# Performance work log

Measured on AMD Instinct MI355X. Metric: run time of the kernel, lower is better.

The kernel has to match this reference:

```python
import jax, jax.numpy as jnp
import numpy as np

DIM, HEADS, DEPTH, SEQ, LOCAL_W = 1024, 16, 7, 2048, 64
HEAD_DIM = DIM // HEADS
SCALE = 1.0 / HEAD_DIM ** 0.5


def cantor_mask(S, depth, local_window):
    """Allowed (i,j): |i-j| within local window, OR |i-j| lies in the Cantor set
    under `depth` levels of ternary subdivision (no base-3 digit equals 1)."""
    idx = np.arange(S)
    d = np.abs(idx[:, None] - idx[None, :])
    x = d.copy()
    ok = np.ones_like(d, dtype=bool)
    for _ in range(depth):
        ok &= (x % 3) != 1
        x //= 3
    ok &= x == 0  # offset must be < 3**depth
    return jnp.asarray(ok | (d <= local_window))  # [S, S] bool


def setup_inputs() -> dict:
    key = jax.random.key(0)
    ks = jax.random.split(key, 8)
    B = 2
    s = 0.02
    return {
        "query": jax.random.normal(ks[0], (B, SEQ, DIM), jnp.float32),
        "key_value": jax.random.normal(ks[1], (B, SEQ, DIM), jnp.float32),
        "Wq": jax.random.normal(ks[2], (DIM, DIM), jnp.float32) * s,
        "bq": jnp.zeros((DIM,), jnp.float32),
        "Wkv": jax.random.normal(ks[3], (DIM, 2 * DIM), jnp.float32) * s,
        "bkv": jnp.zeros((2 * DIM,), jnp.float32),
        "Wo": jax.random.normal(ks[4], (DIM, DIM), jnp.float32) * s,
        "bo": jnp.zeros((DIM,), jnp.float32),
    }


def reference(query, key_value, Wq, bq, Wkv, bkv, Wo, bo):
    B, S, D = query.shape
    H, hd = HEADS, HEAD_DIM
    mask = cantor_mask(S, DEPTH, LOCAL_W)  # static [S, S] bool

    q = (query @ Wq + bq).reshape(B, S, H, hd).transpose(0, 2, 1, 3)  # [B,H,S,hd]
    kv = (key_value @ Wkv + bkv).reshape(B, S, 2, H, hd).transpose(2, 0, 3, 1, 4)
    k, v = kv[0], kv[1]  # [B,H,S,hd]

    scores = jnp.einsum("bhqd,bhkd->bhqk", q, k) * SCALE
    scores = jnp.where(mask, scores, jnp.finfo(scores.dtype).min)
    attn = jax.nn.softmax(scores, axis=-1)
    out = jnp.einsum("bhqk,bhkd->bhqd", attn, v)  # [B,H,S,hd]
    out = out.transpose(0, 2, 1, 3).reshape(B, S, D)
    return out @ Wo + bo
```

## Files before the change

### kernel.cpp

```cpp
#include <hip/hip_runtime.h>
#include <stdint.h>

typedef _Float16 half_t;
typedef __attribute__((ext_vector_type(8))) _Float16 half8;
typedef __attribute__((ext_vector_type(4))) _Float16 half4;
typedef __attribute__((ext_vector_type(4))) float floatx4;

#define SEQ 2048
#define NH 16
#define HD 64

#define MFMA16(a, b, c) __builtin_amdgcn_mfma_f32_16x16x16f16(a, b, c, 0, 0, 0)
#define MFMA32K(a, b, c) __builtin_amdgcn_mfma_f32_16x16x32_f16(a, b, c, 0, 0, 0)

#define QSCALE 0.1803368801111306f

__global__ __launch_bounds__(256) void prep(
    const float* __restrict__ query, const float* __restrict__ key_value,
    const float* __restrict__ Wq, const float* __restrict__ Wkv,
    const float* __restrict__ Wo, half_t* __restrict__ xq,
    half_t* __restrict__ xkv, half_t* __restrict__ wqT,
    half_t* __restrict__ wkvT, half_t* __restrict__ woT,
    uint8_t* __restrict__ tok, uint8_t* __restrict__ tok16,
    uint64_t* __restrict__ maskw) {
  int bx = blockIdx.x, tid = threadIdx.x;
  if (bx < 2048) {
    const float* s; half_t* d; int base;
    if (bx < 1024) { s = query; d = xq; base = bx * 4096; }
    else { s = key_value; d = xkv; base = (bx - 1024) * 4096; }
#pragma unroll
    for (int u = 0; u < 4; ++u) {
      int i = base + u * 1024 + tid * 4;
      floatx4 v = *(const floatx4*)(s + i);
      half4 h;
      h[0] = (half_t)v[0]; h[1] = (half_t)v[1];
      h[2] = (half_t)v[2]; h[3] = (half_t)v[3];
      *(half4*)(d + i) = h;
    }
    return;
  }
  if (bx < 4096) {
    __shared__ float tile[32][33];
    int tx = tid & 31, ty = tid >> 5;
    const int K = 1024;
#pragma unroll
    for (int u = 0; u < 2; ++u) {
      int t = (bx - 2048) * 2 + u;
      const float* W; half_t* Wt; int N, nt, kt;
      if (t < 1024) { W = Wq; Wt = wqT; N = 1024; nt = t & 31; kt = t >> 5; }
      else if (t < 3072) { int t2 = t - 1024; W = Wkv; Wt = wkvT; N = 2048; nt = t2 & 63; kt = t2 >> 6; }
      else { int t2 = t - 3072; W = Wo; Wt = woT; N = 1024; nt = t2 & 31; kt = t2 >> 5; }
      int n0 = nt * 32, k0 = kt * 32;
#pragma unroll
      for (int i = 0; i < 4; ++i)
        tile[ty + i * 8][tx] = W[(size_t)(k0 + ty + i * 8) * N + n0 + tx];
      __syncthreads();
#pragma unroll
      for (int i = 0; i < 4; ++i)
        Wt[(size_t)(n0 + ty + i * 8) * K + k0 + tx] = (half_t)tile[tx][ty + i * 8];
      __syncthreads();
    }
    return;
  }
  __shared__ uint8_t slut[2048];
  int ib = bx - 4096;
  for (int d = tid; d < 2048; d += 256) {
    int x = d;
    bool ok = true;
    for (int it = 0; it < 7; ++it) { ok &= ((x % 3) != 1); x /= 3; }
    ok &= (x == 0);
    slut[d] = (ok || d <= 64) ? 1 : 0;
  }
  __syncthreads();
  if (ib == 0) {
    if (tid < 64) {
      int delta = tid - 32;
      int lo = delta * 64 - 63, hi = delta * 64 + 63;
      uint8_t any = 0;
      for (int x = lo; x <= hi; ++x) {
        int a = x < 0 ? -x : x;
        if (a < 2048) any |= slut[a];
      }
      tok[tid] = any;
    }
    {
      int d16 = tid - 128;
      int ctr = d16 * 16;
      uint8_t any = 0;
      for (int x = ctr - 15; x <= ctr + 15; ++x) {
        int a = x < 0 ? -x : x;
        if (a < 2048) any |= slut[a];
      }
      tok16[tid] = any;
    }
  }
  int g = ib * 256 + tid;
  int tt = g - 2048;
  uint64_t w = 0;
  for (int jj = 0; jj < 64; ++jj) {
    int d = tt - jj; d = d < 0 ? -d : d;
    if (d < 2048 && slut[d]) w |= (1ull << jj);
  }
  maskw[g] = w;
}

__device__ __forceinline__ void cp16(half_t* lds, const half_t* g) {
  __builtin_amdgcn_global_load_lds(
      (const __attribute__((address_space(1))) uint32_t*)g,
      (__attribute__((address_space(3))) uint32_t*)lds, 16, 0, 0);
}

__global__ __launch_bounds__(256) void gemm_qkv(
    const half_t* __restrict__ xq, const half_t* __restrict__ xkv,
    const half_t* __restrict__ wqT, const half_t* __restrict__ wkvT,
    const float* __restrict__ bq, const float* __restrict__ bkv,
    half_t* __restrict__ qout, half_t* __restrict__ kout,
    half_t* __restrict__ vTout) {
  extern __shared__ char smemraw[];
  half_t* As = (half_t*)smemraw;
  half_t* Bs = As + 8192;
  const int K = 1024;
  bool isq = blockIdx.y < 8;
  const half_t* A = isq ? xq : xkv;
  const half_t* Bt = isq ? wqT : wkvT;
  const float* bias = isq ? bq : bkv;
  int n0 = (isq ? blockIdx.y : (blockIdx.y - 8)) * 128;
  int m0 = blockIdx.x * 128;

  int tid = threadIdx.x;
  int wave = tid >> 6, lane = tid & 63;
  int c = lane & 15, quad = lane >> 4;
  int wm = (wave >> 1) * 64, wn = (wave & 1) * 64;

  floatx4 acc[4][4] = {};
  int arow = tid >> 2, akc = (tid & 3) * 8;

  cp16(&As[wave * 512], A + (size_t)(m0 + arow) * K + akc);
  cp16(&As[2048 + wave * 512], A + (size_t)(m0 + 64 + arow) * K + akc);
  cp16(&Bs[wave * 512], Bt + (size_t)(n0 + arow) * K + akc);
  cp16(&Bs[2048 + wave * 512], Bt + (size_t)(n0 + 64 + arow) * K + akc);

  for (int kt = 0; kt < 32; ++kt) {
    __syncthreads();
    if (kt + 1 < 32) {
      int k0 = (kt + 1) * 32;
      int b = (kt + 1) & 1;
      cp16(&As[b * 4096 + wave * 512], A + (size_t)(m0 + arow) * K + k0 + akc);
      cp16(&As[b * 4096 + 2048 + wave * 512], A + (size_t)(m0 + 64 + arow) * K + k0 + akc);
      cp16(&Bs[b * 4096 + wave * 512], Bt + (size_t)(n0 + arow) * K + k0 + akc);
      cp16(&Bs[b * 4096 + 2048 + wave * 512], Bt + (size_t)(n0 + 64 + arow) * K + k0 + akc);
    }
    int b = kt & 1;
    half8 af[4], bf[4];
#pragma unroll
    for (int mt = 0; mt < 4; ++mt)
      af[mt] = *(const half8*)&As[b * 4096 + (wm + mt * 16 + c) * 32 + quad * 8];
#pragma unroll
    for (int nt = 0; nt < 4; ++nt)
      bf[nt] = *(const half8*)&Bs[b * 4096 + (wn + nt * 16 + c) * 32 + quad * 8];
#pragma unroll
    for (int mt = 0; mt < 4; ++mt)
#pragma unroll
      for (int nt = 0; nt < 4; ++nt)
        acc[mt][nt] = MFMA32K(af[mt], bf[nt], acc[mt][nt]);
  }

  __syncthreads();
  half_t* ep = (half_t*)smemraw;
  int bb = m0 >> 11, sbase = m0 & 2047;
  bool isv = (!isq) && (n0 >= 1024);

  if (!isv) {
#pragma unroll
    for (int nt = 0; nt < 4; ++nt) {
      int nl = wn + nt * 16 + c;
      float bv = bias[n0 + nl];
#pragma unroll
      for (int mt = 0; mt < 4; ++mt)
#pragma unroll
        for (int r = 0; r < 4; ++r) {
          int ml = wm + mt * 16 + quad * 4 + r;
          float v = acc[mt][nt][r] + bv;
          if (isq) v *= QSCALE;
          ep[ml * 128 + nl] = (half_t)v;
        }
    }
    __syncthreads();
    half_t* outp = isq ? qout : kout;
#pragma unroll
    for (int rd = 0; rd < 8; ++rd) {
      int id = rd * 256 + tid;
      int ml = id >> 4, ch = id & 15;
      int ng = n0 + ch * 8;
      int h = ng >> 6, d0 = ng & 63;
      half8 v = *(const half8*)&ep[ml * 128 + ch * 8];
      *(half8*)(outp + ((size_t)(bb * 16 + h) * SEQ + sbase + ml) * 64 + d0) = v;
    }
  } else {
#pragma unroll
    for (int nt = 0; nt < 4; ++nt) {
      int nl = wn + nt * 16 + c;
      float bv = bias[n0 + nl];
#pragma unroll
      for (int mt = 0; mt < 4; ++mt) {
        int ml = wm + mt * 16 + quad * 4;
        half4 hv;
#pragma unroll
        for (int r = 0; r < 4; ++r) hv[r] = (half_t)(acc[mt][nt][r] + bv);
        *(half4*)&ep[nl * 136 + ml] = hv;
      }
    }
    __syncthreads();
#pragma unroll
    for (int rd = 0; rd < 8; ++rd) {
      int id = rd * 256 + tid;
      int nl = id >> 4, mc = id & 15;
      int ng = n0 + nl;
      int h = (ng >> 6) & 15, d = ng & 63;
      half8 v = *(const half8*)&ep[nl * 136 + mc * 8];
      *(half8*)(vTout + ((size_t)(bb * 16 + h) * 64 + d) * SEQ + sbase + mc * 8) = v;
    }
  }
}

__global__ __launch_bounds__(256) void gemm_out(
    const half_t* __restrict__ A, const half_t* __restrict__ Bt,
    const float* __restrict__ bias, float* __restrict__ outf) {
  __shared__ half_t As[2][128 * 32];
  __shared__ half_t Bs[2][64 * 32];
  const int K = 1024;
  int tid = threadIdx.x;
  int wave = tid >> 6, lane = tid & 63;
  int c = lane & 15, quad = lane >> 4;
  int wm = (wave >> 1) * 64, wn = (wave & 1) * 32;
  int m0 = blockIdx.x * 128, n0 = blockIdx.y * 64;

  floatx4 acc[4][2] = {};
  int arow = tid >> 2, akc = (tid & 3) * 8;

  cp16(&As[0][wave * 512], A + (size_t)(m0 + arow) * K + akc);
  cp16(&As[0][2048 + wave * 512], A + (size_t)(m0 + 64 + arow) * K + akc);
  cp16(&Bs[0][wave * 512], Bt + (size_t)(n0 + arow) * K + akc);

  for (int kt = 0; kt < 32; ++kt) {
    __syncthreads();
    if (kt + 1 < 32) {
      int k0 = (kt + 1) * 32;
      int b = (kt + 1) & 1;
      cp16(&As[b][wave * 512], A + (size_t)(m0 + arow) * K + k0 + akc);
      cp16(&As[b][2048 + wave * 512], A + (size_t)(m0 + 64 + arow) * K + k0 + akc);
      cp16(&Bs[b][wave * 512], Bt + (size_t)(n0 + arow) * K + k0 + akc);
    }
    int b = kt & 1;
    half8 af[4], bf[2];
#pragma unroll
    for (int mt = 0; mt < 4; ++mt)
      af[mt] = *(const half8*)&As[b][(wm + mt * 16 + c) * 32 + quad * 8];
#pragma unroll
    for (int nt = 0; nt < 2; ++nt)
      bf[nt] = *(const half8*)&Bs[b][(wn + nt * 16 + c) * 32 + quad * 8];
#pragma unroll
    for (int mt = 0; mt < 4; ++mt)
#pragma unroll
      for (int nt = 0; nt < 2; ++nt)
        acc[mt][nt] = MFMA32K(af[mt], bf[nt], acc[mt][nt]);
  }

#pragma unroll
  for (int nt = 0; nt < 2; ++nt) {
    int n = n0 + wn + nt * 16 + c;
    float bv = bias[n];
#pragma unroll
    for (int mt = 0; mt < 4; ++mt)
#pragma unroll
      for (int r = 0; r < 4; ++r) {
        int m = m0 + wm + mt * 16 + quad * 4 + r;
        outf[(size_t)m * 1024 + n] = acc[mt][nt][r] + bv;
      }
  }
}

__global__ __launch_bounds__(512) void attn_kernel(
    const half_t* __restrict__ qb, const half_t* __restrict__ kb,
    const half_t* __restrict__ vTg, half_t* __restrict__ ctx,
    const uint64_t* __restrict__ maskw, const uint8_t* __restrict__ tok,
    const uint8_t* __restrict__ tok16g) {
  __shared__ half_t kT[64 * 64];
  __shared__ half_t vT[64 * 64];
  __shared__ half_t ot[128 * 72];
  __shared__ int list[34];
  __shared__ uint8_t tok16s[256];

  int tid = threadIdx.x, wave = tid >> 6, lane = tid & 63;
  int c = lane & 15, q = lane >> 4;
  int id = blockIdx.x;
  int bh = (id & 7) * 4 + ((id >> 3) & 3);
  int it128 = id >> 5;
  int i0 = it128 << 7;
  const half_t* qbase = qb + (size_t)bh * SEQ * HD;
  const half_t* kg = kb + (size_t)bh * SEQ * HD;
  const half_t* vg = vTg + (size_t)bh * HD * SEQ;

  if (tid < 256) tok16s[tid] = tok16g[tid];
  if (wave == 0) {
    int jt = lane;
    int base = i0 >> 6;
    bool act = (jt < 32) &&
               (tok[(jt - base) + 32] | tok[(jt - base - 1) + 32]);
    unsigned long long bal = __ballot(act);
    if (act) {
      int pre = __popcll(bal & ((1ull << jt) - 1));
      list[1 + pre] = jt << 6;
    }
    if (lane == 0) list[0] = __popcll(bal);
  }

  int i_row = i0 + wave * 16 + c;
  int it16 = (i0 >> 4) + wave;
  half8 qf0 = *(const half8*)(qbase + (size_t)i_row * 64 + q * 8);
  half8 qf1 = *(const half8*)(qbase + (size_t)i_row * 64 + 32 + q * 8);

  floatx4 oacc[4] = {};
  floatx4 lacc = {};
  half4 ones;
  ones[0] = (half_t)1.f; ones[1] = (half_t)1.f;
  ones[2] = (half_t)1.f; ones[3] = (half_t)1.f;

  int srow = tid >> 3;
  int sch = tid & 7;
  int ssw = srow & 7;

  __syncthreads();
  int nact = list[0];
  int j0 = list[1];

  half8 kr = *(const half8*)(kg + (size_t)(j0 + srow) * 64 + sch * 8);
  half8 vr = *(const half8*)(vg + (size_t)srow * SEQ + j0 + sch * 8);

  for (int ti = 0; ti < nact; ++ti) {
    uint64_t w = maskw[(i_row - j0) + 2048];
    int bidx = (j0 >> 4) - it16 + 128;
    __syncthreads();
    *(half8*)&kT[srow * 64 + ((sch ^ ssw) * 8)] = kr;
    *(half8*)&vT[srow * 64 + ((sch ^ ssw) * 8)] = vr;
    int j0n = j0;
    if (ti + 1 < nact) {
      j0n = list[2 + ti];
      kr = *(const half8*)(kg + (size_t)(j0n + srow) * 64 + sch * 8);
      vr = *(const half8*)(vg + (size_t)srow * SEQ + j0n + sch * 8);
    }
    __syncthreads();

    uint32_t wlo = (uint32_t)(w >> (4 * q));
    uint32_t whi = (uint32_t)(w >> (32 + 4 * q));
#pragma unroll
    for (int jt = 0; jt < 4; ++jt) {
      if (!tok16s[bidx + jt]) continue;
      int row = jt * 16 + c;
      int sw = c & 7;
      half8 a0 = *(const half8*)&kT[row * 64 + ((q ^ sw) * 8)];
      half8 a1 = *(const half8*)&kT[row * 64 + (((4 + q) ^ sw) * 8)];
      floatx4 t = {};
      t = MFMA32K(a0, qf0, t);
      t = MFMA32K(a1, qf1, t);
      uint32_t ww = (jt < 2) ? wlo : whi;
#pragma unroll
      for (int r = 0; r < 4; ++r) {
        float p = __builtin_exp2f(t[r]);
        int bitpos = 16 * (jt & 1) + r;
        uint32_t msk = (uint32_t)(((int)(ww << (31 - bitpos))) >> 31);
        t[r] = __uint_as_float(__float_as_uint(p) & msk);
      }
      auto lo = __builtin_amdgcn_cvt_pkrtz(t[0], t[1]);
      auto hi = __builtin_amdgcn_cvt_pkrtz(t[2], t[3]);
      half4 pb;
      pb[0] = lo[0]; pb[1] = lo[1]; pb[2] = hi[0]; pb[3] = hi[1];
      lacc = MFMA16(ones, pb, lacc);
#pragma unroll
      for (int mt = 0; mt < 4; ++mt) {
        int drow = mt * 16 + c;
        int ch = 2 * jt + (q >> 1);
        half4 a = *(const half4*)&vT[drow * 64 + ((ch ^ sw) * 8) + (q & 1) * 4];
        oacc[mt] = MFMA16(a, pb, oacc[mt]);
      }
    }
    j0 = j0n;
  }

  float inv_l = 1.0f / lacc[0];
#pragma unroll
  for (int mt = 0; mt < 4; ++mt)
#pragma unroll
    for (int r = 0; r < 4; ++r)
      ot[(wave * 16 + c) * 72 + mt * 16 + 4 * q + r] = (half_t)(oacc[mt][r] * inv_l);
  __syncthreads();
  {
    int row = tid >> 2, chq = tid & 3;
    int b = bh >> 4, h = bh & 15;
    size_t base = (((size_t)(b * SEQ + i0 + row) * NH) + h) * 64 + chq * 16;
    half8 v0 = *(const half8*)&ot[row * 72 + chq * 16];
    half8 v1 = *(const half8*)&ot[row * 72 + chq * 16 + 8];
    *(half8*)(ctx + base) = v0;
    *(half8*)(ctx + base + 8) = v1;
  }
}

extern "C" void kernel_launch(void* const* d_in, const int* in_sizes, int n_in,
                              void* d_out, int out_size, void* d_ws, size_t ws_size,
                              hipStream_t stream) {
  const float* query = (const float*)d_in[0];
  const float* key_value = (const float*)d_in[1];
  const float* Wq = (const float*)d_in[2];
  const float* bq = (const float*)d_in[3];
  const float* Wkv = (const float*)d_in[4];
  const float* bkv = (const float*)d_in[5];
  const float* Wo = (const float*)d_in[6];
  const float* bo = (const float*)d_in[7];

  char* ws = (char*)d_ws;
  uint8_t* tok = (uint8_t*)ws;
  uint8_t* tok16 = (uint8_t*)(ws + 1024);
  uint64_t* maskw = (uint64_t*)(ws + 4096);
  const size_t MB = 1ull << 20;
  half_t* xq = (half_t*)(ws + 1 * MB);
  half_t* xkv = (half_t*)(ws + 9 * MB);
  half_t* wqT = (half_t*)(ws + 17 * MB);
  half_t* wkvT = (half_t*)(ws + 19 * MB);
  half_t* woT = (half_t*)(ws + 23 * MB);
  half_t* qbuf = (half_t*)(ws + 25 * MB);
  half_t* kbuf = (half_t*)(ws + 33 * MB);
  half_t* vTg = (half_t*)(ws + 41 * MB);
  half_t* ctx = xq;

  hipLaunchKernelGGL(prep, dim3(4112), dim3(256), 0, stream,
                     query, key_value, Wq, Wkv, Wo, xq, xkv, wqT, wkvT, woT,
                     tok, tok16, maskw);
  hipLaunchKernelGGL(gemm_qkv, dim3(32, 24), dim3(256), 34816, stream,
                     xq, xkv, wqT, wkvT, bq, bkv, qbuf, kbuf, vTg);
  hipLaunchKernelGGL(attn_kernel, dim3(512), dim3(512), 0, stream,
                     qbuf, kbuf, vTg, ctx, maskw, tok, tok16);
  hipLaunchKernelGGL(gemm_out, dim3(32, 16), dim3(256), 0, stream,
                     ctx, woT, bo, (float*)d_out);
}
```

Measured before the change: 218.1 us.

## Swizzle GEMM LDS tiles and double-buffer K/V tiles in attention

The two GEMM kernels XOR-swizzle the 16-byte chunk position within each 32-half LDS row, on both the async copy side and the fragment-read side, to reduce LDS bank conflicts. The attention kernel gets two K and V shared-memory buffers and prefetches two tiles ahead in registers. This cuts the per-tile barriers from two to one, so the next tile's LDS store can overlap the current tile's MFMA work. The cost is twice the LDS for K/V (lower occupancy possible) and extra registers for the second prefetch set.

Result: no change. 216.9 us (-0.6%).

```diff
diff --git a/kernel.cpp b/kernel.cpp
--- a/kernel.cpp
+++ b/kernel.cpp
@@ -133,7 +133,9 @@
   int wm = (wave >> 1) * 64, wn = (wave & 1) * 64;
 
   floatx4 acc[4][4] = {};
-  int arow = tid >> 2, akc = (tid & 3) * 8;
+  int arow = tid >> 2;
+  int akc = ((tid & 3) ^ (arow & 3)) * 8;
+  int csw = c & 3;
 
   cp16(&As[wave * 512], A + (size_t)(m0 + arow) * K + akc);
   cp16(&As[2048 + wave * 512], A + (size_t)(m0 + 64 + arow) * K + akc);
@@ -154,10 +156,10 @@
     half8 af[4], bf[4];
 #pragma unroll
     for (int mt = 0; mt < 4; ++mt)
-      af[mt] = *(const half8*)&As[b * 4096 + (wm + mt * 16 + c) * 32 + quad * 8];
+      af[mt] = *(const half8*)&As[b * 4096 + (wm + mt * 16 + c) * 32 + ((quad ^ csw) * 8)];
 #pragma unroll
     for (int nt = 0; nt < 4; ++nt)
-      bf[nt] = *(const half8*)&Bs[b * 4096 + (wn + nt * 16 + c) * 32 + quad * 8];
+      bf[nt] = *(const half8*)&Bs[b * 4096 + (wn + nt * 16 + c) * 32 + ((quad ^ csw) * 8)];
 #pragma unroll
     for (int mt = 0; mt < 4; ++mt)
 #pragma unroll
@@ -236,7 +238,9 @@
   int m0 = blockIdx.x * 128, n0 = blockIdx.y * 64;
 
   floatx4 acc[4][2] = {};
-  int arow = tid >> 2, akc = (tid & 3) * 8;
+  int arow = tid >> 2;
+  int akc = ((tid & 3) ^ (arow & 3)) * 8;
+  int csw = c & 3;
 
   cp16(&As[0][wave * 512], A + (size_t)(m0 + arow) * K + akc);
   cp16(&As[0][2048 + wave * 512], A + (size_t)(m0 + 64 + arow) * K + akc);
@@ -255,10 +259,10 @@
     half8 af[4], bf[2];
 #pragma unroll
     for (int mt = 0; mt < 4; ++mt)
-      af[mt] = *(const half8*)&As[b][(wm + mt * 16 + c) * 32 + quad * 8];
+      af[mt] = *(const half8*)&As[b][(wm + mt * 16 + c) * 32 + ((quad ^ csw) * 8)];
 #pragma unroll
     for (int nt = 0; nt < 2; ++nt)
-      bf[nt] = *(const half8*)&Bs[b][(wn + nt * 16 + c) * 32 + quad * 8];
+      bf[nt] = *(const half8*)&Bs[b][(wn + nt * 16 + c) * 32 + ((quad ^ csw) * 8)];
 #pragma unroll
     for (int mt = 0; mt < 4; ++mt)
 #pragma unroll
@@ -285,8 +289,8 @@
     const half_t* __restrict__ vTg, half_t* __restrict__ ctx,
     const uint64_t* __restrict__ maskw, const uint8_t* __restrict__ tok,
     const uint8_t* __restrict__ tok16g) {
-  __shared__ half_t kT[64 * 64];
-  __shared__ half_t vT[64 * 64];
+  __shared__ half_t kT[2][64 * 64];
+  __shared__ half_t vT[2][64 * 64];
   __shared__ half_t ot[128 * 72];
   __shared__ int list[34];
   __shared__ uint8_t tok16s[256];
@@ -329,28 +333,52 @@
   int srow = tid >> 3;
   int sch = tid & 7;
   int ssw = srow & 7;
+  int sslot = (sch ^ ssw) * 8;
 
   __syncthreads();
   int nact = list[0];
-  int j0 = list[1];
-
-  half8 kr = *(const half8*)(kg + (size_t)(j0 + srow) * 64 + sch * 8);
-  half8 vr = *(const half8*)(vg + (size_t)srow * SEQ + j0 + sch * 8);
+
+  half8 kr0, vr0, kr1, vr1;
+  {
+    int j0 = list[1];
+    kr0 = *(const half8*)(kg + (size_t)(j0 + srow) * 64 + sch * 8);
+    vr0 = *(const half8*)(vg + (size_t)srow * SEQ + j0 + sch * 8);
+    int j1 = (nact > 1) ? list[2] : j0;
+    kr1 = *(const half8*)(kg + (size_t)(j1 + srow) * 64 + sch * 8);
+    vr1 = *(const half8*)(vg + (size_t)srow * SEQ + j1 + sch * 8);
+  }
+  *(half8*)&kT[0][srow * 64 + sslot] = kr0;
+  *(half8*)&vT[0][srow * 64 + sslot] = vr0;
+  __syncthreads();
 
   for (int ti = 0; ti < nact; ++ti) {
-    uint64_t w = maskw[(i_row - j0) + 2048];
-    int bidx = (j0 >> 4) - it16 + 128;
-    __syncthreads();
-    *(half8*)&kT[srow * 64 + ((sch ^ ssw) * 8)] = kr;
-    *(half8*)&vT[srow * 64 + ((sch ^ ssw) * 8)] = vr;
-    int j0n = j0;
+    int cur = ti & 1;
+    int jc = list[1 + ti];
+    uint64_t w = maskw[(i_row - jc) + 2048];
+    int bidx = (jc >> 4) - it16 + 128;
+
     if (ti + 1 < nact) {
-      j0n = list[2 + ti];
-      kr = *(const half8*)(kg + (size_t)(j0n + srow) * 64 + sch * 8);
-      vr = *(const half8*)(vg + (size_t)srow * SEQ + j0n + sch * 8);
-    }
-    __syncthreads();
-
+      if (cur == 0) {
+        *(half8*)&kT[1][srow * 64 + sslot] = kr1;
+        *(half8*)&vT[1][srow * 64 + sslot] = vr1;
+        if (ti + 2 < nact) {
+          int j2 = list[3 + ti];
+          kr0 = *(const half8*)(kg + (size_t)(j2 + srow) * 64 + sch * 8);
+          vr0 = *(const half8*)(vg + (size_t)srow * SEQ + j2 + sch * 8);
+        }
+      } else {
+        *(half8*)&kT[0][srow * 64 + sslot] = kr0;
+        *(half8*)&vT[0][srow * 64 + sslot] = vr0;
+        if (ti + 2 < nact) {
+          int j2 = list[3 + ti];
+          kr1 = *(const half8*)(kg + (size_t)(j2 + srow) * 64 + sch * 8);
+          vr1 = *(const half8*)(vg + (size_t)srow * SEQ + j2 + sch * 8);
+        }
+      }
+    }
+
+    const half_t* kTc = kT[cur];
+    const half_t* vTc = vT[cur];
     uint32_t wlo = (uint32_t)(w >> (4 * q));
     uint32_t whi = (uint32_t)(w >> (32 + 4 * q));
 #pragma unroll
@@ -358,8 +386,8 @@
       if (!tok16s[bidx + jt]) continue;
       int row = jt * 16 + c;
       int sw = c & 7;
-      half8 a0 = *(const half8*)&kT[row * 64 + ((q ^ sw) * 8)];
-      half8 a1 = *(const half8*)&kT[row * 64 + (((4 + q) ^ sw) * 8)];
+      half8 a0 = *(const half8*)&kTc[row * 64 + ((q ^ sw) * 8)];
+      half8 a1 = *(const half8*)&kTc[row * 64 + (((4 + q) ^ sw) * 8)];
       floatx4 t = {};
       t = MFMA32K(a0, qf0, t);
       t = MFMA32K(a1, qf1, t);
@@ -380,11 +408,11 @@
       for (int mt = 0; mt < 4; ++mt) {
         int drow = mt * 16 + c;
         int ch = 2 * jt + (q >> 1);
-        half4 a = *(const half4*)&vT[drow * 64 + ((ch ^ sw) * 8) + (q & 1) * 4];
+        half4 a = *(const half4*)&vTc[drow * 64 + ((ch ^ sw) * 8) + (q & 1) * 4];
         oacc[mt] = MFMA16(a, pb, oacc[mt]);
       }
     }
-    j0 = j0n;
+    __syncthreads();
   }
 
   float inv_l = 1.0f / lacc[0];
```
